# Kernel optimization log

Measured on AMD Instinct MI355X. Metric: run time of the kernel, lower is better.

Reference implementation:

```python
import jax, jax.numpy as jnp
import numpy as np

B, N, M, K, C = 2, 4096, 4096, 32, 64
RADIUS = 0.08


def _ball_query(d2, radius, k):
    # d2: (B, N, M) squared distances. Returns (B, N, k) int32 indices of the
    # first k in-radius neighbors (in index order); empty slots are filled with
    # the first found neighbor (or 0 if none), matching standard ball_query.
    m = d2.shape[-1]
    mask = d2 < radius * radius
    ar = jnp.arange(m, dtype=jnp.int32)
    key = jnp.where(mask, ar, ar + m)          # in-radius indices sort first
    neg_vals, _ = jax.lax.top_k(-key, k)       # k smallest keys
    vals = -neg_vals
    valid = vals < m
    raw = vals % m
    fill = raw[..., :1]                        # first neighbor (0 if none)
    return jnp.where(valid, raw, fill)


def setup_inputs() -> dict:
    key = jax.random.key(0)
    ks = jax.random.split(key, 9)
    points = jax.random.uniform(ks[0], (B, 3, N), dtype=jnp.float32)
    knnpoints = jax.random.uniform(ks[1], (B, 3, M), dtype=jnp.float32)
    feat = jax.random.normal(ks[2], (B, C, M), dtype=jnp.float32)
    w1 = jax.random.normal(ks[3], (128, C + 4), dtype=jnp.float32) * 0.05
    b1 = jnp.zeros((128,), jnp.float32)
    w2 = jax.random.normal(ks[4], (64, 128), dtype=jnp.float32) * 0.05
    b2 = jnp.zeros((64,), jnp.float32)
    w3 = jax.random.normal(ks[5], (64, 64), dtype=jnp.float32) * 0.05
    b3 = jnp.zeros((64,), jnp.float32)
    return {"points": points, "knnpoints": knnpoints, "feat": feat,
            "w1": w1, "b1": b1, "w2": w2, "b2": b2, "w3": w3, "b3": b3}


def reference(points, knnpoints, feat, w1, b1, w2, b2, w3, b3):
    # pairwise squared distances (B, N, M), computed once and reused by
    # ball_query and ChamferLoss
    pe = jnp.sum(points ** 2, axis=1)                       # (B, N)
    ke = jnp.sum(knnpoints ** 2, axis=1)                    # (B, M)
    cross = jnp.einsum('bdn,bdm->bnm', points, knnpoints)
    d2 = jnp.maximum(pe[:, :, None] + ke[:, None, :] - 2.0 * cross, 0.0)

    idx = _ball_query(jax.lax.stop_gradient(d2), RADIUS, K)  # (B, N, K)

    # gather neighbor coords / features: knnpoints[j, :, idx[j]]
    nb = jax.vmap(lambda p, i: p[:, i])(knnpoints, idx)      # (B, 3, N, K)
    nf = jax.vmap(lambda f, i: f[:, i])(feat, idx)           # (B, C, N, K)

    # relation features (neighbor_feature): diff + squared distance
    diff = nb - points[:, :, :, None]                        # (B, 3, N, K)
    dist = jnp.sum(diff ** 2, axis=1, keepdims=True)         # (B, 1, N, K)
    x = jnp.concatenate([nf, diff, dist], axis=1)            # (B, C+4, N, K)

    # SharedMLP: 1x1 conv stacks + ReLU
    h = jax.nn.relu(jnp.einsum('oc,bcnk->bonk', w1, x) + b1[None, :, None, None])
    h = jax.nn.relu(jnp.einsum('oc,bcnk->bonk', w2, h) + b2[None, :, None, None])
    h = jax.nn.relu(jnp.einsum('oc,bcnk->bonk', w3, h) + b3[None, :, None, None])
    agg = jnp.sum(h, axis=3)                                 # (B, 64, N)

    # ChamferLoss between points and knnpoints
    cd = jnp.sqrt(1e-6 + d2)
    loss = jnp.min(cd, axis=1).mean() + jnp.min(cd, axis=2).mean()
    return agg, loss
```

## Files before the change

kernel.cpp:

```cpp
#include <hip/hip_runtime.h>
#include <cstdint>

#define BB 2
#define NN 4096
#define MM 4096
#define KK 32
#define CC 64
#define R2C 0.0064f

typedef _Float16 v8h __attribute__((ext_vector_type(8)));
typedef _Float16 v4h __attribute__((ext_vector_type(4)));
typedef float    v4f __attribute__((ext_vector_type(4)));

#define TC  64
#define XS  104
#define H1S 136
#define H2S 72

__launch_bounds__(256)
__global__ void scan_setup_kernel(const float* __restrict__ points,
                                  const float* __restrict__ knn,
                                  const float* __restrict__ feat,
                                  const float* __restrict__ w1,
                                  const float* __restrict__ w2,
                                  const float* __restrict__ w3,
                                  _Float16* __restrict__ featH,
                                  _Float16* __restrict__ w1h,
                                  _Float16* __restrict__ w2h,
                                  _Float16* __restrict__ w3h,
                                  int* __restrict__ idx_ws,
                                  float* __restrict__ lossbuf) {
    __shared__ __align__(16) char SM[16640];
    __shared__ int sidx[16][KK];
    float4* tile = (float4*)SM;
    int t = threadIdx.x;
    int w = t >> 6, lane = t & 63;
    int blk = blockIdx.x;

    if (blk < 512) {
        int pt0 = blk * 16;
        int b = blk >> 8;
        const float* pp = points + (size_t)b * 3 * NN;
        const float* kp = knn + (size_t)b * 3 * MM;
        float4 P[4];
#pragma unroll
        for (int p = 0; p < 4; ++p) {
            int nl = (pt0 & (NN - 1)) + 4 * w + p;
            float x = pp[nl], y = pp[NN + nl], z = pp[2 * NN + nl];
            float e = __fadd_rn(__fadd_rn(__fmul_rn(x, x), __fmul_rn(y, y)),
                                __fmul_rn(z, z));
            P[p] = make_float4(x, y, z, e);
        }
        int cnt[4] = {0, 0, 0, 0};
        float mn[4] = {1e30f, 1e30f, 1e30f, 1e30f};

        for (int ch = 0; ch < 4; ++ch) {
            const float* kx = kp + ch * 1024;
#pragma unroll
            for (int j = 0; j < 4; ++j) {
                int i = t + 256 * j;
                float x = kx[i], y = kx[MM + i], z = kx[2 * MM + i];
                float e = __fadd_rn(__fadd_rn(__fmul_rn(x, x), __fmul_rn(y, y)),
                                    __fmul_rn(z, z));
                tile[i] = make_float4(x, y, z, e);
            }
            __syncthreads();
#pragma unroll 2
            for (int i = 0; i < 16; ++i) {
                float4 k4 = tile[i * 64 + lane];
                int m = ch * 1024 + i * 64 + lane;
#pragma unroll
                for (int p = 0; p < 4; ++p) {
                    float cross = __builtin_fmaf(P[p].z, k4.z,
                                  __builtin_fmaf(P[p].y, k4.y,
                                                 __fmul_rn(P[p].x, k4.x)));
                    float d2 = __fsub_rn(__fadd_rn(P[p].w, k4.w),
                                         __fmul_rn(2.0f, cross));
                    mn[p] = fminf(mn[p], d2);
                    bool hit = d2 < R2C;
                    unsigned long long mask = __ballot(hit);
                    if (hit) {
                        int pos = cnt[p] + __builtin_amdgcn_mbcnt_hi(
                                     (unsigned)(mask >> 32),
                                     __builtin_amdgcn_mbcnt_lo((unsigned)mask, 0));
                        if (pos < KK) sidx[4 * w + p][pos] = m;
                    }
                    cnt[p] += __popcll(mask);
                }
            }
            __syncthreads();
        }

        float lsum = 0.0f;
#pragma unroll
        for (int p = 0; p < 4; ++p) {
            int row = 4 * w + p;
            if (lane < KK) {
                int fillv = (cnt[p] > 0) ? sidx[row][0] : 0;
                int v = (lane < cnt[p]) ? sidx[row][lane] : fillv;
                idx_ws[((size_t)(pt0 + row)) * KK + lane] = v;
            }
            float mv = mn[p];
            for (int off = 32; off > 0; off >>= 1)
                mv = fminf(mv, __shfl_xor(mv, off));
            lsum += sqrtf(1e-6f + fmaxf(mv, 0.0f));
        }
        if (lane == 0)
            lossbuf[blk * 4 + w] = lsum * (1.0f / (BB * NN));
    } else if (blk < 1024) {
        int blk2 = blk - 512;
        int m0 = blk2 * 16;
        int b = blk2 >> 8;
        const float* pp = points + (size_t)b * 3 * NN;
        const float* kp = knn + (size_t)b * 3 * MM;
        float4 Kp[4];
#pragma unroll
        for (int p = 0; p < 4; ++p) {
            int ml = (m0 & (MM - 1)) + 4 * w + p;
            float x = kp[ml], y = kp[MM + ml], z = kp[2 * MM + ml];
            float e = __fadd_rn(__fadd_rn(__fmul_rn(x, x), __fmul_rn(y, y)),
                                __fmul_rn(z, z));
            Kp[p] = make_float4(x, y, z, e);
        }
        float mn[4] = {1e30f, 1e30f, 1e30f, 1e30f};

        for (int ch = 0; ch < 4; ++ch) {
            const float* px = pp + ch * 1024;
#pragma unroll
            for (int j = 0; j < 4; ++j) {
                int i = t + 256 * j;
                float x = px[i], y = px[NN + i], z = px[2 * NN + i];
                float e = __fadd_rn(__fadd_rn(__fmul_rn(x, x), __fmul_rn(y, y)),
                                    __fmul_rn(z, z));
                tile[i] = make_float4(x, y, z, e);
            }
            __syncthreads();
#pragma unroll 2
            for (int i = 0; i < 16; ++i) {
                float4 p4 = tile[i * 64 + lane];
#pragma unroll
                for (int p = 0; p < 4; ++p) {
                    float cross = __builtin_fmaf(p4.z, Kp[p].z,
                                  __builtin_fmaf(p4.y, Kp[p].y,
                                                 __fmul_rn(p4.x, Kp[p].x)));
                    float d2 = __fsub_rn(__fadd_rn(p4.w, Kp[p].w),
                                         __fmul_rn(2.0f, cross));
                    mn[p] = fminf(mn[p], d2);
                }
            }
            __syncthreads();
        }

        float lsum = 0.0f;
#pragma unroll
        for (int p = 0; p < 4; ++p) {
            float mv = mn[p];
            for (int off = 32; off > 0; off >>= 1)
                mv = fminf(mv, __shfl_xor(mv, off));
            lsum += sqrtf(1e-6f + fmaxf(mv, 0.0f));
        }
        if (lane == 0)
            lossbuf[2048 + blk2 * 4 + w] = lsum * (1.0f / (BB * MM));
    } else if (blk < 1152) {
        float (*tl)[65] = (float (*)[65])SM;
        int tb = blk - 1024;
        int b = tb / (MM / 64);
        int m0 = (tb % (MM / 64)) * 64;
        int mi = t & 63, cq = t >> 6;
        const float* src = feat + (size_t)b * CC * MM;
#pragma unroll
        for (int r = 0; r < 16; ++r) {
            int c = cq * 16 + r;
            tl[mi][c] = src[(size_t)c * MM + m0 + mi];
        }
        __syncthreads();
        int ci = t & 63, mq = t >> 6;
        _Float16* dst = featH + ((size_t)b * MM + m0) * CC;
#pragma unroll
        for (int r = 0; r < 16; ++r) {
            int mm = mq * 16 + r;
            dst[(size_t)mm * CC + ci] = (_Float16)tl[mm][ci];
        }
    } else {
        int tt = (blk - 1152) * 256 + t;
        if (tt < 128 * 96) {
            int r = tt / 96, k = tt - r * 96;
            w1h[tt] = (_Float16)((k < 68) ? w1[r * 68 + k] : 0.0f);
        }
        if (tt < 64 * 128) w2h[tt] = (_Float16)w2[tt];
        if (tt < 64 * 64)  w3h[tt] = (_Float16)w3[tt];
    }
}

__launch_bounds__(256, 4)
__global__ void mlp_kernel(const float* __restrict__ points,
                           const float* __restrict__ knn,
                           const _Float16* __restrict__ featH,
                           const int* __restrict__ idx_ws,
                           const _Float16* __restrict__ w1h, const float* __restrict__ b1,
                           const _Float16* __restrict__ w2h, const float* __restrict__ b2,
                           const _Float16* __restrict__ w3h, const float* __restrict__ b3,
                           const float* __restrict__ lossbuf,
                           float* __restrict__ out) {
    __shared__ __align__(16) _Float16 SM[TC * XS + TC * H1S];
    _Float16* X  = SM;
    _Float16* H2 = SM;
    _Float16* H1 = SM + TC * XS;
    __shared__ float ws4[4];

    int t = threadIdx.x;

    if (blockIdx.x == 0) {
        float s = 0.0f;
#pragma unroll
        for (int q = 0; q < 16; ++q) s += lossbuf[t + 256 * q];
        for (int off = 32; off > 0; off >>= 1) s += __shfl_xor(s, off);
        if ((t & 63) == 0) ws4[t >> 6] = s;
        __syncthreads();
        if (t == 0)
            out[(size_t)BB * 64 * NN] = ws4[0] + ws4[1] + ws4[2] + ws4[3];
    }

    int point0 = blockIdx.x * 2;
    int b = point0 >> 12;
    int n0 = point0 & (NN - 1);
    const float* pp = points + (size_t)b * 3 * NN;
    const float* kp = knn + (size_t)b * 3 * MM;

    {
        int col = t >> 2, h = t & 3;
        int pl = col >> 5, kk = col & 31;
        int n = n0 + pl;
        int id = idx_ws[(((size_t)b * NN + n) << 5) + kk];
        const v8h* src = (const v8h*)(featH + ((size_t)(b * MM + id)) * CC) + h * 2;
        v8h f0 = src[0], f1 = src[1];
        v8h* dst = (v8h*)(X + col * XS) + h * 2;
        dst[0] = f0; dst[1] = f1;
        v8h mv = {(_Float16)0.f, (_Float16)0.f, (_Float16)0.f, (_Float16)0.f,
                  (_Float16)0.f, (_Float16)0.f, (_Float16)0.f, (_Float16)0.f};
        if (h == 0) {
            float px = pp[n], py = pp[NN + n], pz = pp[2 * NN + n];
            float kx = kp[id], ky = kp[MM + id], kz = kp[2 * MM + id];
            float dx = kx - px, dy = ky - py, dz = kz - pz;
            float dd = __fadd_rn(__fadd_rn(__fmul_rn(dx, dx), __fmul_rn(dy, dy)),
                                 __fmul_rn(dz, dz));
            mv[0] = (_Float16)dx; mv[1] = (_Float16)dy;
            mv[2] = (_Float16)dz; mv[3] = (_Float16)dd;
        }
        *((v8h*)(X + col * XS + 64) + h) = mv;
    }

    int w = t >> 6, l = t & 63;
    int quad = l >> 4, lc = l & 15;

    v8h a1[2][3], a2[4], a3[2];
#pragma unroll
    for (int rt = 0; rt < 2; ++rt)
#pragma unroll
        for (int ks = 0; ks < 3; ++ks)
            a1[rt][ks] = *(const v8h*)(w1h + (32 * w + 16 * rt + lc) * 96 + 32 * ks + 8 * quad);
#pragma unroll
    for (int ks = 0; ks < 4; ++ks)
        a2[ks] = *(const v8h*)(w2h + (16 * w + lc) * 128 + 32 * ks + 8 * quad);
#pragma unroll
    for (int ks = 0; ks < 2; ++ks)
        a3[ks] = *(const v8h*)(w3h + (16 * w + lc) * 64 + 32 * ks + 8 * quad);

    v4f bias1a = *(const v4f*)(b1 + 32 * w + 4 * quad);
    v4f bias1b = *(const v4f*)(b1 + 32 * w + 16 + 4 * quad);
    v4f bias2  = *(const v4f*)(b2 + 16 * w + 4 * quad);
    v4f bias3  = *(const v4f*)(b3 + 16 * w + 4 * quad);

    __syncthreads();

#pragma unroll 1
    for (int ct = 0; ct < 4; ++ct) {
        int colb = 16 * ct + lc;
        v4f acc0 = bias1a, acc1 = bias1b;
#pragma unroll
        for (int ks = 0; ks < 3; ++ks) {
            v8h bx = *(const v8h*)(X + colb * XS + 32 * ks + 8 * quad);
            acc0 = __builtin_amdgcn_mfma_f32_16x16x32_f16(a1[0][ks], bx, acc0, 0, 0, 0);
            acc1 = __builtin_amdgcn_mfma_f32_16x16x32_f16(a1[1][ks], bx, acc1, 0, 0, 0);
        }
        v4h h0, h1v;
#pragma unroll
        for (int r = 0; r < 4; ++r) {
            h0[r]  = (_Float16)fmaxf(acc0[r], 0.0f);
            h1v[r] = (_Float16)fmaxf(acc1[r], 0.0f);
        }
        *(v4h*)(H1 + colb * H1S + 32 * w + 4 * quad)      = h0;
        *(v4h*)(H1 + colb * H1S + 32 * w + 16 + 4 * quad) = h1v;
    }
    __syncthreads();

#pragma unroll 1
    for (int ct = 0; ct < 4; ++ct) {
        int colb = 16 * ct + lc;
        v4f acc = bias2;
#pragma unroll
        for (int ks = 0; ks < 4; ++ks) {
            v8h bx = *(const v8h*)(H1 + colb * H1S + 32 * ks + 8 * quad);
            acc = __builtin_amdgcn_mfma_f32_16x16x32_f16(a2[ks], bx, acc, 0, 0, 0);
        }
        v4h h;
#pragma unroll
        for (int r = 0; r < 4; ++r) h[r] = (_Float16)fmaxf(acc[r], 0.0f);
        *(v4h*)(H2 + colb * H2S + 16 * w + 4 * quad) = h;
    }
    __syncthreads();

#pragma unroll 1
    for (int p = 0; p < 2; ++p) {
        int cA = (2 * p) * 16 + lc, cB = (2 * p + 1) * 16 + lc;
        v4f accA = bias3, accB = bias3;
#pragma unroll
        for (int ks = 0; ks < 2; ++ks) {
            v8h bA = *(const v8h*)(H2 + cA * H2S + 32 * ks + 8 * quad);
            v8h bB = *(const v8h*)(H2 + cB * H2S + 32 * ks + 8 * quad);
            accA = __builtin_amdgcn_mfma_f32_16x16x32_f16(a3[ks], bA, accA, 0, 0, 0);
            accB = __builtin_amdgcn_mfma_f32_16x16x32_f16(a3[ks], bB, accB, 0, 0, 0);
        }
        v4f s;
#pragma unroll
        for (int r = 0; r < 4; ++r)
            s[r] = fmaxf(accA[r], 0.0f) + fmaxf(accB[r], 0.0f);
#pragma unroll
        for (int off = 1; off < 16; off <<= 1) {
#pragma unroll
            for (int r = 0; r < 4; ++r) s[r] += __shfl_xor(s[r], off);
        }
        if (lc == 0) {
            int n = n0 + p;
            int rowb = 16 * w + 4 * quad;
#pragma unroll
            for (int r = 0; r < 4; ++r)
                out[((size_t)(b * 64 + rowb + r)) * NN + n] = s[r];
        }
    }
}

extern "C" void kernel_launch(void* const* d_in, const int* in_sizes, int n_in,
                              void* d_out, int out_size, void* d_ws, size_t ws_size,
                              hipStream_t stream) {
    const float* points = (const float*)d_in[0];
    const float* knn    = (const float*)d_in[1];
    const float* feat   = (const float*)d_in[2];
    const float* w1 = (const float*)d_in[3];
    const float* b1 = (const float*)d_in[4];
    const float* w2 = (const float*)d_in[5];
    const float* b2 = (const float*)d_in[6];
    const float* w3 = (const float*)d_in[7];
    const float* b3 = (const float*)d_in[8];
    float* out = (float*)d_out;

    char* ws = (char*)d_ws;
    _Float16*  featH   = (_Float16*)ws;
    int*       idx_ws  = (int*)(ws + 1048576);
    _Float16*  w1h     = (_Float16*)(ws + 2097152);
    _Float16*  w2h     = (_Float16*)(ws + 2121728);
    _Float16*  w3h     = (_Float16*)(ws + 2138112);
    float*     lossbuf = (float*)(ws + 2146304);

    scan_setup_kernel<<<1200, 256, 0, stream>>>(points, knn, feat, w1, w2, w3,
                                                featH, w1h, w2h, w3h,
                                                idx_ws, lossbuf);
    mlp_kernel<<<(BB * NN) / 2, 256, 0, stream>>>(points, knn, featH, idx_ws,
                                                  w1h, b1, w2h, b2, w3h, b3,
                                                  lossbuf, out);
}
```

Measured before the change: 118.8 us.

## Fuse ball-query scan into MLP kernel with precomputed knn float4 table

Moves the per-point ball-query scan and row-min loss into the MLP kernel, so each block scans all M candidates for its two points across four waves, merges the per-wave neighbor lists in shared memory, and feeds them straight to the gather and MFMA stages. This removes the global idx workspace round-trip. A small prep kernel now converts features and weights and precomputes packed (x,y,z,|k|^2) float4s. The column-min blocks share the same launch, and a last-block atomic counter does the final loss reduction. The trade-off is more scan work per block (2 points vs 16), which may lower arithmetic reuse of the knn loads.

```diff
diff --git a/kernel.cpp b/kernel.cpp
--- a/kernel.cpp
+++ b/kernel.cpp
@@ -17,111 +17,101 @@
 #define H1S 136
 #define H2S 72
 
+#define NBLK_COLMIN 512
+#define NBLK_MLP    4096
+#define NBLK_TOTAL  4608
+
 __launch_bounds__(256)
-__global__ void scan_setup_kernel(const float* __restrict__ points,
-                                  const float* __restrict__ knn,
-                                  const float* __restrict__ feat,
-                                  const float* __restrict__ w1,
-                                  const float* __restrict__ w2,
-                                  const float* __restrict__ w3,
-                                  _Float16* __restrict__ featH,
-                                  _Float16* __restrict__ w1h,
-                                  _Float16* __restrict__ w2h,
-                                  _Float16* __restrict__ w3h,
-                                  int* __restrict__ idx_ws,
-                                  float* __restrict__ lossbuf) {
-    __shared__ __align__(16) char SM[16640];
-    __shared__ int sidx[16][KK];
-    float4* tile = (float4*)SM;
+__global__ void prep_kernel(const float* __restrict__ knn,
+                            const float* __restrict__ feat,
+                            const float* __restrict__ w1,
+                            const float* __restrict__ w2,
+                            const float* __restrict__ w3,
+                            _Float16* __restrict__ featH,
+                            _Float16* __restrict__ w1h,
+                            _Float16* __restrict__ w2h,
+                            _Float16* __restrict__ w3h,
+                            float4* __restrict__ knnP,
+                            int* __restrict__ ctr) {
+    __shared__ __align__(16) float tl[64][65];
+    int t = threadIdx.x, blk = blockIdx.x;
+    if (blk == 0 && t == 0) *ctr = 0;
+
+    if (blk < 128) {
+        int b = blk >> 6;
+        int m0 = (blk & 63) * 64;
+        int mi = t & 63, cq = t >> 6;
+        const float* src = feat + (size_t)b * CC * MM;
+#pragma unroll
+        for (int r = 0; r < 16; ++r) {
+            int c = cq * 16 + r;
+            tl[mi][c] = src[(size_t)c * MM + m0 + mi];
+        }
+        __syncthreads();
+        int ci = t & 63, mq = t >> 6;
+        _Float16* dst = featH + ((size_t)b * MM + m0) * CC;
+#pragma unroll
+        for (int r = 0; r < 16; ++r) {
+            int mm2 = mq * 16 + r;
+            dst[(size_t)mm2 * CC + ci] = (_Float16)tl[mm2][ci];
+        }
+    } else if (blk < 176) {
+        int tt = (blk - 128) * 256 + t;
+        if (tt < 128 * 96) {
+            int r = tt / 96, k = tt - r * 96;
+            w1h[tt] = (_Float16)((k < 68) ? w1[r * 68 + k] : 0.0f);
+        }
+        if (tt < 64 * 128) w2h[tt] = (_Float16)w2[tt];
+        if (tt < 64 * 64)  w3h[tt] = (_Float16)w3[tt];
+    } else {
+        int i0 = (blk - 176) * 256 + t;
+#pragma unroll
+        for (int j = 0; j < 4; ++j) {
+            int i = i0 + 2048 * j;
+            int b = i >> 12, m = i & (MM - 1);
+            const float* kp = knn + (size_t)b * 3 * MM;
+            float x = kp[m], y = kp[MM + m], z = kp[2 * MM + m];
+            float e = __fadd_rn(__fadd_rn(__fmul_rn(x, x), __fmul_rn(y, y)),
+                                __fmul_rn(z, z));
+            knnP[i] = make_float4(x, y, z, e);
+        }
+    }
+}
+
+__launch_bounds__(256, 4)
+__global__ void fused_kernel(const float* __restrict__ points,
+                             const float4* __restrict__ knnP,
+                             const _Float16* __restrict__ featH,
+                             const _Float16* __restrict__ w1h, const float* __restrict__ b1,
+                             const _Float16* __restrict__ w2h, const float* __restrict__ b2,
+                             const _Float16* __restrict__ w3h, const float* __restrict__ b3,
+                             float* __restrict__ lossbuf,
+                             int* __restrict__ ctr,
+                             float* __restrict__ out) {
+    __shared__ __align__(16) _Float16 SM[TC * XS + TC * H1S];
+    _Float16* X  = SM;
+    _Float16* H2 = SM;
+    _Float16* H1 = SM + TC * XS;
+    __shared__ int   lists[2][4][KK];
+    __shared__ int   cnts[2][4];
+    __shared__ int   sidx2[2][KK];
+    __shared__ float wmin[2][4];
+    __shared__ int   sLast;
+
     int t = threadIdx.x;
     int w = t >> 6, lane = t & 63;
     int blk = blockIdx.x;
 
-    if (blk < 512) {
-        int pt0 = blk * 16;
+    if (blk < NBLK_COLMIN) {
+        float4* tile = (float4*)SM;
+        int m0 = blk * 16;
         int b = blk >> 8;
         const float* pp = points + (size_t)b * 3 * NN;
-        const float* kp = knn + (size_t)b * 3 * MM;
-        float4 P[4];
-#pragma unroll
-        for (int p = 0; p < 4; ++p) {
-            int nl = (pt0 & (NN - 1)) + 4 * w + p;
-            float x = pp[nl], y = pp[NN + nl], z = pp[2 * NN + nl];
-            float e = __fadd_rn(__fadd_rn(__fmul_rn(x, x), __fmul_rn(y, y)),
-                                __fmul_rn(z, z));
-            P[p] = make_float4(x, y, z, e);
-        }
-        int cnt[4] = {0, 0, 0, 0};
-        float mn[4] = {1e30f, 1e30f, 1e30f, 1e30f};
-
-        for (int ch = 0; ch < 4; ++ch) {
-            const float* kx = kp + ch * 1024;
-#pragma unroll
-            for (int j = 0; j < 4; ++j) {
-                int i = t + 256 * j;
-                float x = kx[i], y = kx[MM + i], z = kx[2 * MM + i];
-                float e = __fadd_rn(__fadd_rn(__fmul_rn(x, x), __fmul_rn(y, y)),
-                                    __fmul_rn(z, z));
-                tile[i] = make_float4(x, y, z, e);
-            }
-            __syncthreads();
-#pragma unroll 2
-            for (int i = 0; i < 16; ++i) {
-                float4 k4 = tile[i * 64 + lane];
-                int m = ch * 1024 + i * 64 + lane;
-#pragma unroll
-                for (int p = 0; p < 4; ++p) {
-                    float cross = __builtin_fmaf(P[p].z, k4.z,
-                                  __builtin_fmaf(P[p].y, k4.y,
-                                                 __fmul_rn(P[p].x, k4.x)));
-                    float d2 = __fsub_rn(__fadd_rn(P[p].w, k4.w),
-                                         __fmul_rn(2.0f, cross));
-                    mn[p] = fminf(mn[p], d2);
-                    bool hit = d2 < R2C;
-                    unsigned long long mask = __ballot(hit);
-                    if (hit) {
-                        int pos = cnt[p] + __builtin_amdgcn_mbcnt_hi(
-                                     (unsigned)(mask >> 32),
-                                     __builtin_amdgcn_mbcnt_lo((unsigned)mask, 0));
-                        if (pos < KK) sidx[4 * w + p][pos] = m;
-                    }
-                    cnt[p] += __popcll(mask);
-                }
-            }
-            __syncthreads();
-        }
-
-        float lsum = 0.0f;
-#pragma unroll
-        for (int p = 0; p < 4; ++p) {
-            int row = 4 * w + p;
-            if (lane < KK) {
-                int fillv = (cnt[p] > 0) ? sidx[row][0] : 0;
-                int v = (lane < cnt[p]) ? sidx[row][lane] : fillv;
-                idx_ws[((size_t)(pt0 + row)) * KK + lane] = v;
-            }
-            float mv = mn[p];
-            for (int off = 32; off > 0; off >>= 1)
-                mv = fminf(mv, __shfl_xor(mv, off));
-            lsum += sqrtf(1e-6f + fmaxf(mv, 0.0f));
-        }
-        if (lane == 0)
-            lossbuf[blk * 4 + w] = lsum * (1.0f / (BB * NN));
-    } else if (blk < 1024) {
-        int blk2 = blk - 512;
-        int m0 = blk2 * 16;
-        int b = blk2 >> 8;
-        const float* pp = points + (size_t)b * 3 * NN;
-        const float* kp = knn + (size_t)b * 3 * MM;
+        const float4* kq = knnP + (size_t)b * MM;
         float4 Kp[4];
 #pragma unroll
-        for (int p = 0; p < 4; ++p) {
-            int ml = (m0 & (MM - 1)) + 4 * w + p;
-            float x = kp[ml], y = kp[MM + ml], z = kp[2 * MM + ml];
-            float e = __fadd_rn(__fadd_rn(__fmul_rn(x, x), __fmul_rn(y, y)),
-                                __fmul_rn(z, z));
-            Kp[p] = make_float4(x, y, z, e);
-        }
+        for (int p = 0; p < 4; ++p)
+            Kp[p] = kq[(m0 & (MM - 1)) + 4 * w + p];
         float mn[4] = {1e30f, 1e30f, 1e30f, 1e30f};
 
         for (int ch = 0; ch < 4; ++ch) {
@@ -159,184 +149,218 @@
                 mv = fminf(mv, __shfl_xor(mv, off));
             lsum += sqrtf(1e-6f + fmaxf(mv, 0.0f));
         }
-        if (lane == 0)
-            lossbuf[2048 + blk2 * 4 + w] = lsum * (1.0f / (BB * MM));
-    } else if (blk < 1152) {
-        float (*tl)[65] = (float (*)[65])SM;
-        int tb = blk - 1024;
-        int b = tb / (MM / 64);
-        int m0 = (tb % (MM / 64)) * 64;
-        int mi = t & 63, cq = t >> 6;
-        const float* src = feat + (size_t)b * CC * MM;
-#pragma unroll
-        for (int r = 0; r < 16; ++r) {
-            int c = cq * 16 + r;
-            tl[mi][c] = src[(size_t)c * MM + m0 + mi];
-        }
-        __syncthreads();
-        int ci = t & 63, mq = t >> 6;
-        _Float16* dst = featH + ((size_t)b * MM + m0) * CC;
-#pragma unroll
-        for (int r = 0; r < 16; ++r) {
-            int mm = mq * 16 + r;
-            dst[(size_t)mm * CC + ci] = (_Float16)tl[mm][ci];
-        }
+        if (lane == 0) wmin[0][w] = lsum;
+        __syncthreads();
+        if (t == 0)
+            lossbuf[blk] = (wmin[0][0] + wmin[0][1] + wmin[0][2] + wmin[0][3])
+                           * (1.0f / (BB * MM));
     } else {
-        int tt = (blk - 1152) * 256 + t;
-        if (tt < 128 * 96) {
-            int r = tt / 96, k = tt - r * 96;
-            w1h[tt] = (_Float16)((k < 68) ? w1[r * 68 + k] : 0.0f);
-        }
-        if (tt < 64 * 128) w2h[tt] = (_Float16)w2[tt];
-        if (tt < 64 * 64)  w3h[tt] = (_Float16)w3[tt];
+        int point0 = (blk - NBLK_COLMIN) * 2;
+        int b = point0 >> 12;
+        int n0 = point0 & (NN - 1);
+        const float* pp = points + (size_t)b * 3 * NN;
+        const float4* kq = knnP + (size_t)b * MM;
+
+        float4 P[2];
+#pragma unroll
+        for (int p = 0; p < 2; ++p) {
+            int n = n0 + p;
+            float x = pp[n], y = pp[NN + n], z = pp[2 * NN + n];
+            float e = __fadd_rn(__fadd_rn(__fmul_rn(x, x), __fmul_rn(y, y)),
+                                __fmul_rn(z, z));
+            P[p] = make_float4(x, y, z, e);
+        }
+        int cnt[2] = {0, 0};
+        float mn[2] = {1e30f, 1e30f};
+        int mbase = w * 1024 + lane;
+#pragma unroll 4
+        for (int it = 0; it < 16; ++it) {
+            int m = mbase + it * 64;
+            float4 k4 = kq[m];
+#pragma unroll
+            for (int p = 0; p < 2; ++p) {
+                float cross = __builtin_fmaf(P[p].z, k4.z,
+                              __builtin_fmaf(P[p].y, k4.y,
+                                             __fmul_rn(P[p].x, k4.x)));
+                float d2 = __fsub_rn(__fadd_rn(P[p].w, k4.w),
+                                     __fmul_rn(2.0f, cross));
+                mn[p] = fminf(mn[p], d2);
+                bool hit = d2 < R2C;
+                unsigned long long mask = __ballot(hit);
+                if (hit) {
+                    int pos = cnt[p] + __builtin_amdgcn_mbcnt_hi(
+                                 (unsigned)(mask >> 32),
+                                 __builtin_amdgcn_mbcnt_lo((unsigned)mask, 0));
+                    if (pos < KK) lists[p][w][pos] = m;
+                }
+                cnt[p] += __popcll(mask);
+            }
+        }
+#pragma unroll
+        for (int p = 0; p < 2; ++p) {
+            if (lane == 0) cnts[p][w] = cnt[p];
+            float mv = mn[p];
+            for (int off = 32; off > 0; off >>= 1)
+                mv = fminf(mv, __shfl_xor(mv, off));
+            if (lane == 0) wmin[p][w] = mv;
+        }
+        __syncthreads();
+
+        if (w == 0) {
+            int p = lane >> 5, k = lane & 31;
+            int c0 = cnts[p][0], c1 = cnts[p][1], c2 = cnts[p][2], c3 = cnts[p][3];
+            int o1 = c0, o2 = o1 + c1, o3 = o2 + c2, total = o3 + c3;
+            int fillv = 0;
+            if (c0 > 0)      fillv = lists[p][0][0];
+            else if (c1 > 0) fillv = lists[p][1][0];
+            else if (c2 > 0) fillv = lists[p][2][0];
+            else if (c3 > 0) fillv = lists[p][3][0];
+            int src, base;
+            if (k < o1)      { src = 0; base = 0;  }
+            else if (k < o2) { src = 1; base = o1; }
+            else if (k < o3) { src = 2; base = o2; }
+            else             { src = 3; base = o3; }
+            int v = (k < total) ? lists[p][src][k - base] : fillv;
+            sidx2[p][k] = v;
+            if (lane == 0) {
+                float r0 = fminf(fminf(wmin[0][0], wmin[0][1]),
+                                 fminf(wmin[0][2], wmin[0][3]));
+                float r1 = fminf(fminf(wmin[1][0], wmin[1][1]),
+                                 fminf(wmin[1][2], wmin[1][3]));
+                lossbuf[blk] = (sqrtf(1e-6f + fmaxf(r0, 0.0f)) +
+                                sqrtf(1e-6f + fmaxf(r1, 0.0f)))
+                               * (1.0f / (BB * NN));
+            }
+        }
+        __syncthreads();
+
+        {
+            int col = t >> 2, h = t & 3;
+            int pl = col >> 5, kk = col & 31;
+            int n = n0 + pl;
+            int id = sidx2[pl][kk];
+            const v8h* src = (const v8h*)(featH + ((size_t)(b * MM + id)) * CC) + h * 2;
+            v8h f0 = src[0], f1 = src[1];
+            v8h* dst = (v8h*)(X + col * XS) + h * 2;
+            dst[0] = f0; dst[1] = f1;
+            v8h mv = {(_Float16)0.f, (_Float16)0.f, (_Float16)0.f, (_Float16)0.f,
+                      (_Float16)0.f, (_Float16)0.f, (_Float16)0.f, (_Float16)0.f};
+            if (h == 0) {
+                float4 Pm = pl ? P[1] : P[0];
+                float4 k4 = kq[id];
+                float dx = k4.x - Pm.x, dy = k4.y - Pm.y, dz = k4.z - Pm.z;
+                float dd = __fadd_rn(__fadd_rn(__fmul_rn(dx, dx), __fmul_rn(dy, dy)),
+                                     __fmul_rn(dz, dz));
+                mv[0] = (_Float16)dx; mv[1] = (_Float16)dy;
+                mv[2] = (_Float16)dz; mv[3] = (_Float16)dd;
+            }
+            *((v8h*)(X + col * XS + 64) + h) = mv;
+        }
+
+        int quad = lane >> 4, lc = lane & 15;
+
+        v8h a1[2][3], a2[4], a3[2];
+#pragma unroll
+        for (int rt = 0; rt < 2; ++rt)
+#pragma unroll
+            for (int ks = 0; ks < 3; ++ks)
+                a1[rt][ks] = *(const v8h*)(w1h + (32 * w + 16 * rt + lc) * 96 + 32 * ks + 8 * quad);
+#pragma unroll
+        for (int ks = 0; ks < 4; ++ks)
+            a2[ks] = *(const v8h*)(w2h + (16 * w + lc) * 128 + 32 * ks + 8 * quad);
+#pragma unroll
+        for (int ks = 0; ks < 2; ++ks)
+            a3[ks] = *(const v8h*)(w3h + (16 * w + lc) * 64 + 32 * ks + 8 * quad);
+
+        v4f bias1a = *(const v4f*)(b1 + 32 * w + 4 * quad);
+        v4f bias1b = *(const v4f*)(b1 + 32 * w + 16 + 4 * quad);
+        v4f bias2  = *(const v4f*)(b2 + 16 * w + 4 * quad);
+        v4f bias3  = *(const v4f*)(b3 + 16 * w + 4 * quad);
+
+        __syncthreads();
+
+#pragma unroll 1
+        for (int ct = 0; ct < 4; ++ct) {
+            int colb = 16 * ct + lc;
+            v4f acc0 = bias1a, acc1 = bias1b;
+#pragma unroll
+            for (int ks = 0; ks < 3; ++ks) {
+                v8h bx = *(const v8h*)(X + colb * XS + 32 * ks + 8 * quad);
+                acc0 = __builtin_amdgcn_mfma_f32_16x16x32_f16(a1[0][ks], bx, acc0, 0, 0, 0);
+                acc1 = __builtin_amdgcn_mfma_f32_16x16x32_f16(a1[1][ks], bx, acc1, 0, 0, 0);
+            }
+            v4h h0, h1v;
+#pragma unroll
+            for (int r = 0; r < 4; ++r) {
+                h0[r]  = (_Float16)fmaxf(acc0[r], 0.0f);
+                h1v[r] = (_Float16)fmaxf(acc1[r], 0.0f);
+            }
+            *(v4h*)(H1 + colb * H1S + 32 * w + 4 * quad)      = h0;
+            *(v4h*)(H1 + colb * H1S + 32 * w + 16 + 4 * quad) = h1v;
+        }
+        __syncthreads();
+
+#pragma unroll 1
+        for (int ct = 0; ct < 4; ++ct) {
+            int colb = 16 * ct + lc;
+            v4f acc = bias2;
+#pragma unroll
+            for (int ks = 0; ks < 4; ++ks) {
+                v8h bx = *(const v8h*)(H1 + colb * H1S + 32 * ks + 8 * quad);
+                acc = __builtin_amdgcn_mfma_f32_16x16x32_f16(a2[ks], bx, acc, 0, 0, 0);
+            }
+            v4h h;
+#pragma unroll
+            for (int r = 0; r < 4; ++r) h[r] = (_Float16)fmaxf(acc[r], 0.0f);
+            *(v4h*)(H2 + colb * H2S + 16 * w + 4 * quad) = h;
+        }
+        __syncthreads();
+
+#pragma unroll 1
+        for (int p = 0; p < 2; ++p) {
+            int cA = (2 * p) * 16 + lc, cB = (2 * p + 1) * 16 + lc;
+            v4f accA = bias3, accB = bias3;
+#pragma unroll
+            for (int ks = 0; ks < 2; ++ks) {
+                v8h bA = *(const v8h*)(H2 + cA * H2S + 32 * ks + 8 * quad);
+                v8h bB = *(const v8h*)(H2 + cB * H2S + 32 * ks + 8 * quad);
+                accA = __builtin_amdgcn_mfma_f32_16x16x32_f16(a3[ks], bA, accA, 0, 0, 0);
+                accB = __builtin_amdgcn_mfma_f32_16x16x32_f16(a3[ks], bB, accB, 0, 0, 0);
+            }
+            v4f s;
+#pragma unroll
+            for (int r = 0; r < 4; ++r)
+                s[r] = fmaxf(accA[r], 0.0f) + fmaxf(accB[r], 0.0f);
+#pragma unroll
+            for (int off = 1; off < 16; off <<= 1) {
+#pragma unroll
+                for (int r = 0; r < 4; ++r) s[r] += __shfl_xor(s[r], off);
+            }
+            if (lc == 0) {
+                int n = n0 + p;
+                int rowb = 16 * w + 4 * quad;
+#pragma unroll
+                for (int r = 0; r < 4; ++r)
+                    out[((size_t)(b * 64 + rowb + r)) * NN + n] = s[r];
+            }
+        }
     }
-}
-
-__launch_bounds__(256, 4)
-__global__ void mlp_kernel(const float* __restrict__ points,
-                           const float* __restrict__ knn,
-                           const _Float16* __restrict__ featH,
-                           const int* __restrict__ idx_ws,
-                           const _Float16* __restrict__ w1h, const float* __restrict__ b1,
-                           const _Float16* __restrict__ w2h, const float* __restrict__ b2,
-                           const _Float16* __restrict__ w3h, const float* __restrict__ b3,
-                           const float* __restrict__ lossbuf,
-                           float* __restrict__ out) {
-    __shared__ __align__(16) _Float16 SM[TC * XS + TC * H1S];
-    _Float16* X  = SM;
-    _Float16* H2 = SM;
-    _Float16* H1 = SM + TC * XS;
-    __shared__ float ws4[4];
-
-    int t = threadIdx.x;
-
-    if (blockIdx.x == 0) {
-        float s = 0.0f;
-#pragma unroll
-        for (int q = 0; q < 16; ++q) s += lossbuf[t + 256 * q];
-        for (int off = 32; off > 0; off >>= 1) s += __shfl_xor(s, off);
-        if ((t & 63) == 0) ws4[t >> 6] = s;
-        __syncthreads();
-        if (t == 0)
-            out[(size_t)BB * 64 * NN] = ws4[0] + ws4[1] + ws4[2] + ws4[3];
-    }
-
-    int point0 = blockIdx.x * 2;
-    int b = point0 >> 12;
-    int n0 = point0 & (NN - 1);
-    const float* pp = points + (size_t)b * 3 * NN;
-    const float* kp = knn + (size_t)b * 3 * MM;
-
-    {
-        int col = t >> 2, h = t & 3;
-        int pl = col >> 5, kk = col & 31;
-        int n = n0 + pl;
-        int id = idx_ws[(((size_t)b * NN + n) << 5) + kk];
-        const v8h* src = (const v8h*)(featH + ((size_t)(b * MM + id)) * CC) + h * 2;
-        v8h f0 = src[0], f1 = src[1];
-        v8h* dst = (v8h*)(X + col * XS) + h * 2;
-        dst[0] = f0; dst[1] = f1;
-        v8h mv = {(_Float16)0.f, (_Float16)0.f, (_Float16)0.f, (_Float16)0.f,
-                  (_Float16)0.f, (_Float16)0.f, (_Float16)0.f, (_Float16)0.f};
-        if (h == 0) {
-            float px = pp[n], py = pp[NN + n], pz = pp[2 * NN + n];
-            float kx = kp[id], ky = kp[MM + id], kz = kp[2 * MM + id];
-            float dx = kx - px, dy = ky - py, dz = kz - pz;
-            float dd = __fadd_rn(__fadd_rn(__fmul_rn(dx, dx), __fmul_rn(dy, dy)),
-                                 __fmul_rn(dz, dz));
-            mv[0] = (_Float16)dx; mv[1] = (_Float16)dy;
-            mv[2] = (_Float16)dz; mv[3] = (_Float16)dd;
-        }
-        *((v8h*)(X + col * XS + 64) + h) = mv;
-    }
-
-    int w = t >> 6, l = t & 63;
-    int quad = l >> 4, lc = l & 15;
-
-    v8h a1[2][3], a2[4], a3[2];
-#pragma unroll
-    for (int rt = 0; rt < 2; ++rt)
-#pragma unroll
-        for (int ks = 0; ks < 3; ++ks)
-            a1[rt][ks] = *(const v8h*)(w1h + (32 * w + 16 * rt + lc) * 96 + 32 * ks + 8 * quad);
-#pragma unroll
-    for (int ks = 0; ks < 4; ++ks)
-        a2[ks] = *(const v8h*)(w2h + (16 * w + lc) * 128 + 32 * ks + 8 * quad);
-#pragma unroll
-    for (int ks = 0; ks < 2; ++ks)
-        a3[ks] = *(const v8h*)(w3h + (16 * w + lc) * 64 + 32 * ks + 8 * quad);
-
-    v4f bias1a = *(const v4f*)(b1 + 32 * w + 4 * quad);
-    v4f bias1b = *(const v4f*)(b1 + 32 * w + 16 + 4 * quad);
-    v4f bias2  = *(const v4f*)(b2 + 16 * w + 4 * quad);
-    v4f bias3  = *(const v4f*)(b3 + 16 * w + 4 * quad);
-
-    __syncthreads();
-
-#pragma unroll 1
-    for (int ct = 0; ct < 4; ++ct) {
-        int colb = 16 * ct + lc;
-        v4f acc0 = bias1a, acc1 = bias1b;
-#pragma unroll
-        for (int ks = 0; ks < 3; ++ks) {
-            v8h bx = *(const v8h*)(X + colb * XS + 32 * ks + 8 * quad);
-            acc0 = __builtin_amdgcn_mfma_f32_16x16x32_f16(a1[0][ks], bx, acc0, 0, 0, 0);
-            acc1 = __builtin_amdgcn_mfma_f32_16x16x32_f16(a1[1][ks], bx, acc1, 0, 0, 0);
-        }
-        v4h h0, h1v;
-#pragma unroll
-        for (int r = 0; r < 4; ++r) {
-            h0[r]  = (_Float16)fmaxf(acc0[r], 0.0f);
-            h1v[r] = (_Float16)fmaxf(acc1[r], 0.0f);
-        }
-        *(v4h*)(H1 + colb * H1S + 32 * w + 4 * quad)      = h0;
-        *(v4h*)(H1 + colb * H1S + 32 * w + 16 + 4 * quad) = h1v;
+
+    if (t == 0) {
+        __threadfence();
+        sLast = (atomicAdd(ctr, 1) == NBLK_TOTAL - 1) ? 1 : 0;
     }
     __syncthreads();
-
-#pragma unroll 1
-    for (int ct = 0; ct < 4; ++ct) {
-        int colb = 16 * ct + lc;
-        v4f acc = bias2;
-#pragma unroll
-        for (int ks = 0; ks < 4; ++ks) {
-            v8h bx = *(const v8h*)(H1 + colb * H1S + 32 * ks + 8 * quad);
-            acc = __builtin_amdgcn_mfma_f32_16x16x32_f16(a2[ks], bx, acc, 0, 0, 0);
-        }
-        v4h h;
-#pragma unroll
-        for (int r = 0; r < 4; ++r) h[r] = (_Float16)fmaxf(acc[r], 0.0f);
-        *(v4h*)(H2 + colb * H2S + 16 * w + 4 * quad) = h;
-    }
-    __syncthreads();
-
-#pragma unroll 1
-    for (int p = 0; p < 2; ++p) {
-        int cA = (2 * p) * 16 + lc, cB = (2 * p + 1) * 16 + lc;
-        v4f accA = bias3, accB = bias3;
-#pragma unroll
-        for (int ks = 0; ks < 2; ++ks) {
-            v8h bA = *(const v8h*)(H2 + cA * H2S + 32 * ks + 8 * quad);
-            v8h bB = *(const v8h*)(H2 + cB * H2S + 32 * ks + 8 * quad);
-            accA = __builtin_amdgcn_mfma_f32_16x16x32_f16(a3[ks], bA, accA, 0, 0, 0);
-            accB = __builtin_amdgcn_mfma_f32_16x16x32_f16(a3[ks], bB, accB, 0, 0, 0);
-        }
-        v4f s;
-#pragma unroll
-        for (int r = 0; r < 4; ++r)
-            s[r] = fmaxf(accA[r], 0.0f) + fmaxf(accB[r], 0.0f);
-#pragma unroll
-        for (int off = 1; off < 16; off <<= 1) {
-#pragma unroll
-            for (int r = 0; r < 4; ++r) s[r] += __shfl_xor(s[r], off);
-        }
-        if (lc == 0) {
-            int n = n0 + p;
-            int rowb = 16 * w + 4 * quad;
-#pragma unroll
-            for (int r = 0; r < 4; ++r)
-                out[((size_t)(b * 64 + rowb + r)) * NN + n] = s[r];
-        }
+    if (sLast) {
+        float s = 0.0f;
+#pragma unroll
+        for (int q = 0; q < 18; ++q)
+            s += lossbuf[t + 256 * q];
+        for (int off = 32; off > 0; off >>= 1) s += __shfl_xor(s, off);
+        if (lane == 0) wmin[0][w] = s;
+        __syncthreads();
+        if (t == 0)
+            out[(size_t)BB * 64 * NN] = wmin[0][0] + wmin[0][1] + wmin[0][2] + wmin[0][3];
     }
 }
 
@@ -356,16 +380,16 @@
 
     char* ws = (char*)d_ws;
     _Float16*  featH   = (_Float16*)ws;
-    int*       idx_ws  = (int*)(ws + 1048576);
-    _Float16*  w1h     = (_Float16*)(ws + 2097152);
-    _Float16*  w2h     = (_Float16*)(ws + 2121728);
-    _Float16*  w3h     = (_Float16*)(ws + 2138112);
-    float*     lossbuf = (float*)(ws + 2146304);
-
-    scan_setup_kernel<<<1200, 256, 0, stream>>>(points, knn, feat, w1, w2, w3,
-                                                featH, w1h, w2h, w3h,
-                                                idx_ws, lossbuf);
-    mlp_kernel<<<(BB * NN) / 2, 256, 0, stream>>>(points, knn, featH, idx_ws,
-                                                  w1h, b1, w2h, b2, w3h, b3,
-                                                  lossbuf, out);
+    _Float16*  w1h     = (_Float16*)(ws + 1048576);
+    _Float16*  w2h     = (_Float16*)(ws + 1073152);
+    _Float16*  w3h     = (_Float16*)(ws + 1089536);
+    float4*    knnP    = (float4*)(ws + 1097728);
+    float*     lossbuf = (float*)(ws + 1228800);
+    int*       ctr     = (int*)(ws + 1247232);
+
+    prep_kernel<<<184, 256, 0, stream>>>(knn, feat, w1, w2, w3,
+                                         featH, w1h, w2h, w3h, knnP, ctr);
+    fused_kernel<<<NBLK_TOTAL, 256, 0, stream>>>(points, knnP, featH,
+                                                 w1h, b1, w2h, b2, w3h, b3,
+                                                 lossbuf, ctr, out);
 }
```

Measured after the change: 256.9 us. 116% more time.
